# Performance work log

Hardware: AMD Instinct MI355X
Metric: run time of the kernel (lower is better)

## Reference

```python
import jax, jax.numpy as jnp
import numpy as np

NUM_FIELDS = 39
PER_FIELD_VOCAB = 10000
TOTAL_VOCAB = NUM_FIELDS * PER_FIELD_VOCAB
EMBED_DIM = 128
DIM_INT = (2, 3)
RANKS = (128, 128)
BATCH = 2048


def setup_inputs() -> dict:
    key = jax.random.key(0)
    k_x, k_emb, k_lin, k_b, k_w0, k_w1 = jax.random.split(key, 6)
    x = jax.random.randint(k_x, (BATCH, NUM_FIELDS), 0, PER_FIELD_VOCAB, dtype=jnp.int64 if jax.config.jax_enable_x64 else jnp.int32)
    embed_table = jax.random.normal(k_emb, (TOTAL_VOCAB, EMBED_DIM), dtype=jnp.float32) * 0.01
    linear_table = jax.random.normal(k_lin, (TOTAL_VOCAB, 1), dtype=jnp.float32) * 0.01
    bias = jnp.zeros((1,), dtype=jnp.float32)
    # trunc_normal_(std=0.01) approximated by scaled normal (same distribution family)
    W0 = jax.random.normal(k_w0, (DIM_INT[0], RANKS[0], NUM_FIELDS), dtype=jnp.float32) * 0.01
    W1 = jax.random.normal(k_w1, (DIM_INT[1], RANKS[1], NUM_FIELDS), dtype=jnp.float32) * 0.01
    return {"x": x, "embed_table": embed_table, "linear_table": linear_table,
            "bias": bias, "W0": W0, "W1": W1}


def _calc_cross(emb, W):
    # emb: [B, F, D]; W: [L, R, F]
    # dot_products[b,d,r,l] = sum_f W[l,r,f] * emb[b,f,d]   (torch: 'bljk,bki->bijl')
    dp = jnp.einsum('lrf,bfd->bdrl', W, emb)          # [B, D, R, L]
    prod_over_l = jnp.prod(dp, axis=3)                # [B, D, R]
    return jnp.sum(prod_over_l, axis=(1, 2))[:, None]  # [B, 1]


def reference(x, embed_table, linear_table, bias, W0, W1):
    # per-field offsets into the flat embedding table (FeaturesEmbedding behavior)
    offsets = (jnp.arange(NUM_FIELDS) * PER_FIELD_VOCAB).astype(x.dtype)
    idx = x + offsets[None, :]                        # [B, F]
    emb = embed_table[idx]                            # [B, F, D]
    # FeaturesLinear: sum of per-feature weights + bias -> [B, 1]
    ret = jnp.sum(linear_table[idx], axis=1) + bias
    for W in (W0, W1):
        ret = ret + _calc_cross(emb, W)
    return (ret, 0)
```

## Files before the change

kernel.cpp:

```cpp
#include <hip/hip_runtime.h>
#include <hip/hip_bf16.h>

#define NUM_FIELDS 39
#define PER_FIELD_VOCAB 10000
#define EMBED_DIM 128
#define KPAD 64
#define NL 5
#define RANK 128
#define BATCH 2048
#define LDS_STRIDE 72

typedef __bf16  bf16x8  __attribute__((ext_vector_type(8)));
typedef float   f32x4   __attribute__((ext_vector_type(4)));

__global__ __launch_bounds__(256) void prep_w(const float* __restrict__ W0,
                                              const float* __restrict__ W1,
                                              __bf16* __restrict__ Wb) {
    int i = blockIdx.x * 256 + threadIdx.x;
    if (i >= NL * RANK * KPAD) return;
    int f = i & (KPAD - 1);
    int r = (i >> 6) & (RANK - 1);
    int l = i >> 13;
    float v = 0.f;
    if (f < NUM_FIELDS) {
        if (l < 2) v = W0[(l * RANK + r) * NUM_FIELDS + f];
        else       v = W1[((l - 2) * RANK + r) * NUM_FIELDS + f];
    }
    Wb[i] = (__bf16)v;
}

__global__ __launch_bounds__(256) void tfm_main(const int* __restrict__ x,
                                                const float* __restrict__ embed_table,
                                                const float* __restrict__ linear_table,
                                                const float* __restrict__ bias,
                                                const __bf16* __restrict__ Wb,
                                                float* __restrict__ out,
                                                int out_size) {
    __shared__ int   sidx[NUM_FIELDS];
    __shared__ __align__(16) __bf16 eT[EMBED_DIM * LDS_STRIDE];
    __shared__ float wpart[4];

    const int tid = threadIdx.x;
    const int b   = blockIdx.x;

    if (tid < NUM_FIELDS)
        sidx[tid] = x[b * NUM_FIELDS + tid] + tid * PER_FIELD_VOCAB;
    __syncthreads();

    for (int k = tid; k < NUM_FIELDS * EMBED_DIM; k += 256) {
        int f = k >> 7, d = k & (EMBED_DIM - 1);
        float v = embed_table[(long)sidx[f] * EMBED_DIM + d];
        eT[d * LDS_STRIDE + f] = (__bf16)v;
    }
    for (int k = tid; k < (KPAD - NUM_FIELDS) * EMBED_DIM; k += 256) {
        int f = NUM_FIELDS + (k >> 7), d = k & (EMBED_DIM - 1);
        eT[d * LDS_STRIDE + f] = (__bf16)0.f;
    }

    float partial = 0.f;
    if (tid < NUM_FIELDS) partial = linear_table[sidx[tid]];

    __syncthreads();

    const int wave = tid >> 6, lane = tid & 63;
    const int m = lane & 15, quad = lane >> 4;

    for (int rti = 0; rti < 2; ++rti) {
        const int r0 = (wave * 2 + rti) * 16;
        bf16x8 afrag[NL][2];
#pragma unroll
        for (int l = 0; l < NL; ++l)
#pragma unroll
            for (int kc = 0; kc < 2; ++kc)
                afrag[l][kc] = *reinterpret_cast<const bf16x8*>(
                    &Wb[((size_t)(l * RANK) + r0 + m) * KPAD + kc * 32 + quad * 8]);

        for (int dt = 0; dt < 8; ++dt) {
            const int d0 = dt * 16;
            bf16x8 bfrag[2];
#pragma unroll
            for (int kc = 0; kc < 2; ++kc)
                bfrag[kc] = *reinterpret_cast<const bf16x8*>(
                    &eT[(d0 + m) * LDS_STRIDE + kc * 32 + quad * 8]);

            f32x4 acc[NL];
#pragma unroll
            for (int l = 0; l < NL; ++l) {
                acc[l] = (f32x4){0.f, 0.f, 0.f, 0.f};
#pragma unroll
                for (int kc = 0; kc < 2; ++kc)
                    acc[l] = __builtin_amdgcn_mfma_f32_16x16x32_bf16(
                        afrag[l][kc], bfrag[kc], acc[l], 0, 0, 0);
            }
#pragma unroll
            for (int i = 0; i < 4; ++i)
                partial += acc[0][i] * acc[1][i] + acc[2][i] * acc[3][i] * acc[4][i];
        }
    }

#pragma unroll
    for (int off = 32; off > 0; off >>= 1)
        partial += __shfl_down(partial, off, 64);
    if (lane == 0) wpart[wave] = partial;
    __syncthreads();
    if (tid == 0)
        out[b] = wpart[0] + wpart[1] + wpart[2] + wpart[3] + bias[0];

    if (b == 0)
        for (int j = BATCH + tid; j < out_size; j += 256)
            out[j] = 0.f;
}

extern "C" void kernel_launch(void* const* d_in, const int* in_sizes, int n_in,
                              void* d_out, int out_size, void* d_ws, size_t ws_size,
                              hipStream_t stream) {
    const int*   x            = (const int*)d_in[0];
    const float* embed_table  = (const float*)d_in[1];
    const float* linear_table = (const float*)d_in[2];
    const float* bias         = (const float*)d_in[3];
    const float* W0           = (const float*)d_in[4];
    const float* W1           = (const float*)d_in[5];
    __bf16*      Wb           = (__bf16*)d_ws;

    prep_w<<<(NL * RANK * KPAD + 255) / 256, 256, 0, stream>>>(W0, W1, Wb);
    tfm_main<<<BATCH, 256, 0, stream>>>(x, embed_table, linear_table, bias, Wb,
                                        (float*)d_out, out_size);
}
```

Before: 277.2 us.

## Replace order-2 cross term with Gram matrix contracted against precomputed W0 pair matrix

The L=2 cross term is rewritten algebraically: sum over d,r of the two projections equals the sum over field pairs of the embedding Gram matrix (E E^T) weighted by M01 = W0[0]^T W0[1]. The prep kernel now computes M01 once, and the main kernel builds the 48x48 Gram matrix per sample with MFMA instead of two rank-128 projection GEMMs. This removes 2 of the 5 projection MFMAs per tile. The cost is an extra row-major copy of the embeddings in LDS and per-lane global loads of M01.

```diff
diff --git a/kernel.cpp b/kernel.cpp
--- a/kernel.cpp
+++ b/kernel.cpp
@@ -5,28 +5,41 @@
 #define PER_FIELD_VOCAB 10000
 #define EMBED_DIM 128
 #define KPAD 64
-#define NL 5
+#define NT 3
 #define RANK 128
 #define BATCH 2048
-#define LDS_STRIDE 72
+#define ET_STRIDE 72
+#define E_STRIDE 144
+#define FPAD 48
 
 typedef __bf16  bf16x8  __attribute__((ext_vector_type(8)));
 typedef float   f32x4   __attribute__((ext_vector_type(4)));
 
-__global__ __launch_bounds__(256) void prep_w(const float* __restrict__ W0,
-                                              const float* __restrict__ W1,
-                                              __bf16* __restrict__ Wb) {
-    int i = blockIdx.x * 256 + threadIdx.x;
-    if (i >= NL * RANK * KPAD) return;
-    int f = i & (KPAD - 1);
-    int r = (i >> 6) & (RANK - 1);
-    int l = i >> 13;
-    float v = 0.f;
-    if (f < NUM_FIELDS) {
-        if (l < 2) v = W0[(l * RANK + r) * NUM_FIELDS + f];
-        else       v = W1[((l - 2) * RANK + r) * NUM_FIELDS + f];
+__global__ __launch_bounds__(256) void prep(const float* __restrict__ W0,
+                                            const float* __restrict__ W1,
+                                            __bf16* __restrict__ Wb,
+                                            float* __restrict__ M01) {
+    int blk = blockIdx.x;
+    if (blk < 96) {
+        int i = blk * 256 + threadIdx.x;
+        int f = i & (KPAD - 1);
+        int r = (i >> 6) & (RANK - 1);
+        int l = i >> 13;
+        float v = (f < NUM_FIELDS) ? W1[(l * RANK + r) * NUM_FIELDS + f] : 0.f;
+        Wb[i] = (__bf16)v;
+    } else {
+        int j = (blk - 96) * 256 + threadIdx.x;
+        if (j < FPAD * FPAD) {
+            int f0 = j / FPAD, f1 = j % FPAD;
+            float s = 0.f;
+            if (f0 < NUM_FIELDS && f1 < NUM_FIELDS) {
+#pragma unroll 8
+                for (int r = 0; r < RANK; ++r)
+                    s += W0[r * NUM_FIELDS + f0] * W0[(RANK + r) * NUM_FIELDS + f1];
+            }
+            M01[j] = s;
+        }
     }
-    Wb[i] = (__bf16)v;
 }
 
 __global__ __launch_bounds__(256) void tfm_main(const int* __restrict__ x,
@@ -34,10 +47,12 @@
                                                 const float* __restrict__ linear_table,
                                                 const float* __restrict__ bias,
                                                 const __bf16* __restrict__ Wb,
+                                                const float* __restrict__ M01,
                                                 float* __restrict__ out,
                                                 int out_size) {
     __shared__ int   sidx[NUM_FIELDS];
-    __shared__ __align__(16) __bf16 eT[EMBED_DIM * LDS_STRIDE];
+    __shared__ __align__(16) __bf16 eT[EMBED_DIM * ET_STRIDE];
+    __shared__ __align__(16) __bf16 e [FPAD * E_STRIDE];
     __shared__ float wpart[4];
 
     const int tid = threadIdx.x;
@@ -49,12 +64,18 @@
 
     for (int k = tid; k < NUM_FIELDS * EMBED_DIM; k += 256) {
         int f = k >> 7, d = k & (EMBED_DIM - 1);
-        float v = embed_table[(long)sidx[f] * EMBED_DIM + d];
-        eT[d * LDS_STRIDE + f] = (__bf16)v;
+        float v = embed_table[(size_t)sidx[f] * EMBED_DIM + d];
+        __bf16 bv = (__bf16)v;
+        eT[d * ET_STRIDE + f] = bv;
+        e [f * E_STRIDE  + d] = bv;
     }
     for (int k = tid; k < (KPAD - NUM_FIELDS) * EMBED_DIM; k += 256) {
         int f = NUM_FIELDS + (k >> 7), d = k & (EMBED_DIM - 1);
-        eT[d * LDS_STRIDE + f] = (__bf16)0.f;
+        eT[d * ET_STRIDE + f] = (__bf16)0.f;
+    }
+    for (int k = tid; k < (FPAD - NUM_FIELDS) * EMBED_DIM; k += 256) {
+        int f = NUM_FIELDS + (k >> 7), d = k & (EMBED_DIM - 1);
+        e[f * E_STRIDE + d] = (__bf16)0.f;
     }
 
     float partial = 0.f;
@@ -65,38 +86,60 @@
     const int wave = tid >> 6, lane = tid & 63;
     const int m = lane & 15, quad = lane >> 4;
 
+    bf16x8 afrag[2][NT][2];
+#pragma unroll
     for (int rti = 0; rti < 2; ++rti) {
         const int r0 = (wave * 2 + rti) * 16;
-        bf16x8 afrag[NL][2];
 #pragma unroll
-        for (int l = 0; l < NL; ++l)
+        for (int l = 0; l < NT; ++l)
 #pragma unroll
             for (int kc = 0; kc < 2; ++kc)
-                afrag[l][kc] = *reinterpret_cast<const bf16x8*>(
+                afrag[rti][l][kc] = *reinterpret_cast<const bf16x8*>(
                     &Wb[((size_t)(l * RANK) + r0 + m) * KPAD + kc * 32 + quad * 8]);
+    }
 
-        for (int dt = 0; dt < 8; ++dt) {
-            const int d0 = dt * 16;
-            bf16x8 bfrag[2];
+    float triplep = 0.f;
+    for (int dt = 0; dt < 8; ++dt) {
+        bf16x8 bfrag[2];
 #pragma unroll
-            for (int kc = 0; kc < 2; ++kc)
-                bfrag[kc] = *reinterpret_cast<const bf16x8*>(
-                    &eT[(d0 + m) * LDS_STRIDE + kc * 32 + quad * 8]);
-
-            f32x4 acc[NL];
+        for (int kc = 0; kc < 2; ++kc)
+            bfrag[kc] = *reinterpret_cast<const bf16x8*>(
+                &eT[(dt * 16 + m) * ET_STRIDE + kc * 32 + quad * 8]);
 #pragma unroll
-            for (int l = 0; l < NL; ++l) {
+        for (int rti = 0; rti < 2; ++rti) {
+            f32x4 acc[NT];
+#pragma unroll
+            for (int l = 0; l < NT; ++l) {
                 acc[l] = (f32x4){0.f, 0.f, 0.f, 0.f};
 #pragma unroll
                 for (int kc = 0; kc < 2; ++kc)
                     acc[l] = __builtin_amdgcn_mfma_f32_16x16x32_bf16(
-                        afrag[l][kc], bfrag[kc], acc[l], 0, 0, 0);
+                        afrag[rti][l][kc], bfrag[kc], acc[l], 0, 0, 0);
             }
 #pragma unroll
             for (int i = 0; i < 4; ++i)
-                partial += acc[0][i] * acc[1][i] + acc[2][i] * acc[3][i] * acc[4][i];
+                triplep += acc[0][i] * acc[1][i] * acc[2][i];
         }
     }
+
+    float pairp = 0.f;
+    for (int t = wave; t < 9; t += 4) {
+        const int ti = t / 3, tj = t % 3;
+        f32x4 g = (f32x4){0.f, 0.f, 0.f, 0.f};
+#pragma unroll
+        for (int kc = 0; kc < 4; ++kc) {
+            bf16x8 ga = *reinterpret_cast<const bf16x8*>(
+                &e[(ti * 16 + m) * E_STRIDE + kc * 32 + quad * 8]);
+            bf16x8 gb = *reinterpret_cast<const bf16x8*>(
+                &e[(tj * 16 + m) * E_STRIDE + kc * 32 + quad * 8]);
+            g = __builtin_amdgcn_mfma_f32_16x16x32_bf16(ga, gb, g, 0, 0, 0);
+        }
+#pragma unroll
+        for (int i = 0; i < 4; ++i)
+            pairp += g[i] * M01[(ti * 16 + quad * 4 + i) * FPAD + tj * 16 + m];
+    }
+
+    partial += triplep + pairp;
 
 #pragma unroll
     for (int off = 32; off > 0; off >>= 1)
@@ -120,9 +163,10 @@
     const float* bias         = (const float*)d_in[3];
     const float* W0           = (const float*)d_in[4];
     const float* W1           = (const float*)d_in[5];
-    __bf16*      Wb           = (__bf16*)d_ws;
+    __bf16* Wb  = (__bf16*)d_ws;
+    float*  M01 = (float*)((char*)d_ws + 49152);
 
-    prep_w<<<(NL * RANK * KPAD + 255) / 256, 256, 0, stream>>>(W0, W1, Wb);
-    tfm_main<<<BATCH, 256, 0, stream>>>(x, embed_table, linear_table, bias, Wb,
+    prep<<<96 + 9, 256, 0, stream>>>(W0, W1, Wb, M01);
+    tfm_main<<<BATCH, 256, 0, stream>>>(x, embed_table, linear_table, bias, Wb, M01,
                                         (float*)d_out, out_size);
 }
```

After: 311.2 us. 1.12x slower.

## Fuse weight conversion into main kernel and swizzle packed embedding LDS stores

Applied to the files above, without the earlier changes.

Removes the separate prep_w launch: each block now loads fp32 W0/W1 rows straight from global and converts them to bf16 fragments in registers. The embedding gather is restructured so each thread gathers four fields and writes a packed bf16x4 into an XOR-style swizzled LDS layout, which also zero-fills the padding in the same pass. The cross computation is split into separate W0 (pair) and W1 (triple) passes to lower register pressure, and launch bounds now request 6 blocks per CU. The cost is that every block repeats the weight conversion with unaligned scalar/vector loads instead of reading a precomputed bf16 buffer.

```diff
diff --git a/kernel.cpp b/kernel.cpp
--- a/kernel.cpp
+++ b/kernel.cpp
@@ -4,40 +4,44 @@
 #define NUM_FIELDS 39
 #define PER_FIELD_VOCAB 10000
 #define EMBED_DIM 128
-#define KPAD 64
-#define NL 5
 #define RANK 128
 #define BATCH 2048
-#define LDS_STRIDE 72
+#define ET_STRIDE 72
 
-typedef __bf16  bf16x8  __attribute__((ext_vector_type(8)));
-typedef float   f32x4   __attribute__((ext_vector_type(4)));
+typedef __bf16 bf16x8 __attribute__((ext_vector_type(8)));
+typedef __bf16 bf16x4 __attribute__((ext_vector_type(4)));
+typedef float  f32x4  __attribute__((ext_vector_type(4)));
+typedef float  f32x4u __attribute__((ext_vector_type(4), aligned(4)));
+typedef float  f32x2u __attribute__((ext_vector_type(2), aligned(4)));
 
-__global__ __launch_bounds__(256) void prep_w(const float* __restrict__ W0,
-                                              const float* __restrict__ W1,
-                                              __bf16* __restrict__ Wb) {
-    int i = blockIdx.x * 256 + threadIdx.x;
-    if (i >= NL * RANK * KPAD) return;
-    int f = i & (KPAD - 1);
-    int r = (i >> 6) & (RANK - 1);
-    int l = i >> 13;
-    float v = 0.f;
-    if (f < NUM_FIELDS) {
-        if (l < 2) v = W0[(l * RANK + r) * NUM_FIELDS + f];
-        else       v = W1[((l - 2) * RANK + r) * NUM_FIELDS + f];
+__device__ inline bf16x8 load_afrag(const float* __restrict__ Wrow, int quad, int kc) {
+    if (kc == 0) {
+        f32x4u a = *reinterpret_cast<const f32x4u*>(Wrow + quad * 8);
+        f32x4u b = *reinterpret_cast<const f32x4u*>(Wrow + quad * 8 + 4);
+        return (bf16x8){(__bf16)a[0], (__bf16)a[1], (__bf16)a[2], (__bf16)a[3],
+                        (__bf16)b[0], (__bf16)b[1], (__bf16)b[2], (__bf16)b[3]};
     }
-    Wb[i] = (__bf16)v;
+    if (quad == 0) {
+        f32x4u a = *reinterpret_cast<const f32x4u*>(Wrow + 32);
+        f32x2u b = *reinterpret_cast<const f32x2u*>(Wrow + 36);
+        float  c = Wrow[38];
+        return (bf16x8){(__bf16)a[0], (__bf16)a[1], (__bf16)a[2], (__bf16)a[3],
+                        (__bf16)b[0], (__bf16)b[1], (__bf16)c, (__bf16)0.f};
+    }
+    return (bf16x8){(__bf16)0.f, (__bf16)0.f, (__bf16)0.f, (__bf16)0.f,
+                    (__bf16)0.f, (__bf16)0.f, (__bf16)0.f, (__bf16)0.f};
 }
 
-__global__ __launch_bounds__(256) void tfm_main(const int* __restrict__ x,
-                                                const float* __restrict__ embed_table,
-                                                const float* __restrict__ linear_table,
-                                                const float* __restrict__ bias,
-                                                const __bf16* __restrict__ Wb,
-                                                float* __restrict__ out,
-                                                int out_size) {
-    __shared__ int   sidx[NUM_FIELDS];
-    __shared__ __align__(16) __bf16 eT[EMBED_DIM * LDS_STRIDE];
+__global__ __launch_bounds__(256, 6) void tfm_fused(const int* __restrict__ x,
+                                                    const float* __restrict__ embed_table,
+                                                    const float* __restrict__ linear_table,
+                                                    const float* __restrict__ bias,
+                                                    const float* __restrict__ W0,
+                                                    const float* __restrict__ W1,
+                                                    float* __restrict__ out,
+                                                    int out_size) {
+    __shared__ int sidx[NUM_FIELDS];
+    __shared__ __align__(16) __bf16 eT[EMBED_DIM * ET_STRIDE];
     __shared__ float wpart[4];
 
     const int tid = threadIdx.x;
@@ -47,56 +51,96 @@
         sidx[tid] = x[b * NUM_FIELDS + tid] + tid * PER_FIELD_VOCAB;
     __syncthreads();
 
-    for (int k = tid; k < NUM_FIELDS * EMBED_DIM; k += 256) {
-        int f = k >> 7, d = k & (EMBED_DIM - 1);
-        float v = embed_table[(long)sidx[f] * EMBED_DIM + d];
-        eT[d * LDS_STRIDE + f] = (__bf16)v;
-    }
-    for (int k = tid; k < (KPAD - NUM_FIELDS) * EMBED_DIM; k += 256) {
-        int f = NUM_FIELDS + (k >> 7), d = k & (EMBED_DIM - 1);
-        eT[d * LDS_STRIDE + f] = (__bf16)0.f;
+#pragma unroll
+    for (int i = 0; i < 8; ++i) {
+        int k  = tid + i * 256;
+        int d  = k & (EMBED_DIM - 1);
+        int fq = k >> 7;
+        float v[4];
+#pragma unroll
+        for (int c = 0; c < 4; ++c) {
+            int f = fq * 4 + c;
+            v[c] = (f < NUM_FIELDS) ? embed_table[(size_t)sidx[f] * EMBED_DIM + d] : 0.f;
+        }
+        bf16x4 pk = {(__bf16)v[0], (__bf16)v[1], (__bf16)v[2], (__bf16)v[3]};
+        int fg  = fq >> 1;
+        int grp = (fg + 2 * d) & 7;
+        *reinterpret_cast<bf16x4*>(reinterpret_cast<char*>(eT)
+            + d * (ET_STRIDE * 2) + grp * 16 + (fq & 1) * 8) = pk;
     }
 
-    float partial = 0.f;
-    if (tid < NUM_FIELDS) partial = linear_table[sidx[tid]];
-
+    float partial = (tid < NUM_FIELDS) ? linear_table[sidx[tid]] : 0.f;
     __syncthreads();
 
     const int wave = tid >> 6, lane = tid & 63;
     const int m = lane & 15, quad = lane >> 4;
 
+    float pairp = 0.f, trip = 0.f;
+
     for (int rti = 0; rti < 2; ++rti) {
-        const int r0 = (wave * 2 + rti) * 16;
-        bf16x8 afrag[NL][2];
+        const int r = (wave * 2 + rti) * 16 + m;
+
+        {
+            bf16x8 af[2][2];
 #pragma unroll
-        for (int l = 0; l < NL; ++l)
-#pragma unroll
-            for (int kc = 0; kc < 2; ++kc)
-                afrag[l][kc] = *reinterpret_cast<const bf16x8*>(
-                    &Wb[((size_t)(l * RANK) + r0 + m) * KPAD + kc * 32 + quad * 8]);
-
-        for (int dt = 0; dt < 8; ++dt) {
-            const int d0 = dt * 16;
-            bf16x8 bfrag[2];
-#pragma unroll
-            for (int kc = 0; kc < 2; ++kc)
-                bfrag[kc] = *reinterpret_cast<const bf16x8*>(
-                    &eT[(d0 + m) * LDS_STRIDE + kc * 32 + quad * 8]);
-
-            f32x4 acc[NL];
-#pragma unroll
-            for (int l = 0; l < NL; ++l) {
-                acc[l] = (f32x4){0.f, 0.f, 0.f, 0.f};
+            for (int l = 0; l < 2; ++l) {
+                const float* Wrow = W0 + ((size_t)(l * RANK) + r) * NUM_FIELDS;
 #pragma unroll
                 for (int kc = 0; kc < 2; ++kc)
-                    acc[l] = __builtin_amdgcn_mfma_f32_16x16x32_bf16(
-                        afrag[l][kc], bfrag[kc], acc[l], 0, 0, 0);
+                    af[l][kc] = load_afrag(Wrow, quad, kc);
             }
+            for (int dt = 0; dt < 8; ++dt) {
+                const int d = dt * 16 + m;
+                bf16x8 bfrag[2];
 #pragma unroll
-            for (int i = 0; i < 4; ++i)
-                partial += acc[0][i] * acc[1][i] + acc[2][i] * acc[3][i] * acc[4][i];
+                for (int kc = 0; kc < 2; ++kc) {
+                    int grp = ((kc * 4 + quad) + 2 * d) & 7;
+                    bfrag[kc] = *reinterpret_cast<const bf16x8*>(
+                        reinterpret_cast<const char*>(eT) + d * (ET_STRIDE * 2) + grp * 16);
+                }
+                f32x4 a0 = {0.f, 0.f, 0.f, 0.f}, a1 = {0.f, 0.f, 0.f, 0.f};
+#pragma unroll
+                for (int kc = 0; kc < 2; ++kc) {
+                    a0 = __builtin_amdgcn_mfma_f32_16x16x32_bf16(af[0][kc], bfrag[kc], a0, 0, 0, 0);
+                    a1 = __builtin_amdgcn_mfma_f32_16x16x32_bf16(af[1][kc], bfrag[kc], a1, 0, 0, 0);
+                }
+#pragma unroll
+                for (int i = 0; i < 4; ++i) pairp += a0[i] * a1[i];
+            }
+        }
+
+        {
+            bf16x8 ag[3][2];
+#pragma unroll
+            for (int l = 0; l < 3; ++l) {
+                const float* Wrow = W1 + ((size_t)(l * RANK) + r) * NUM_FIELDS;
+#pragma unroll
+                for (int kc = 0; kc < 2; ++kc)
+                    ag[l][kc] = load_afrag(Wrow, quad, kc);
+            }
+            for (int dt = 0; dt < 8; ++dt) {
+                const int d = dt * 16 + m;
+                bf16x8 bfrag[2];
+#pragma unroll
+                for (int kc = 0; kc < 2; ++kc) {
+                    int grp = ((kc * 4 + quad) + 2 * d) & 7;
+                    bfrag[kc] = *reinterpret_cast<const bf16x8*>(
+                        reinterpret_cast<const char*>(eT) + d * (ET_STRIDE * 2) + grp * 16);
+                }
+                f32x4 a2 = {0.f, 0.f, 0.f, 0.f}, a3 = {0.f, 0.f, 0.f, 0.f}, a4 = {0.f, 0.f, 0.f, 0.f};
+#pragma unroll
+                for (int kc = 0; kc < 2; ++kc) {
+                    a2 = __builtin_amdgcn_mfma_f32_16x16x32_bf16(ag[0][kc], bfrag[kc], a2, 0, 0, 0);
+                    a3 = __builtin_amdgcn_mfma_f32_16x16x32_bf16(ag[1][kc], bfrag[kc], a3, 0, 0, 0);
+                    a4 = __builtin_amdgcn_mfma_f32_16x16x32_bf16(ag[2][kc], bfrag[kc], a4, 0, 0, 0);
+                }
+#pragma unroll
+                for (int i = 0; i < 4; ++i) trip += a2[i] * a3[i] * a4[i];
+            }
         }
     }
+
+    partial += pairp + trip;
 
 #pragma unroll
     for (int off = 32; off > 0; off >>= 1)
@@ -120,9 +164,7 @@
     const float* bias         = (const float*)d_in[3];
     const float* W0           = (const float*)d_in[4];
     const float* W1           = (const float*)d_in[5];
-    __bf16*      Wb           = (__bf16*)d_ws;
 
-    prep_w<<<(NL * RANK * KPAD + 255) / 256, 256, 0, stream>>>(W0, W1, Wb);
-    tfm_main<<<BATCH, 256, 0, stream>>>(x, embed_table, linear_table, bias, Wb,
-                                        (float*)d_out, out_size);
+    tfm_fused<<<BATCH, 256, 0, stream>>>(x, embed_table, linear_table, bias, W0, W1,
+                                         (float*)d_out, out_size);
 }
```

Measured after the change: 488.2 us. 76.1% more time.

## Swizzle transposed embedding LDS layout and pack four fields per store

Applied to the files above, without the earlier changes.

Rewrites the gather-and-transpose into LDS so each thread loads four fields for one embedding dimension and writes them as a packed bf16x4, with an XOR-style group swizzle on the row layout to avoid bank conflicts, and folds the zero padding into the same loop. The MFMA loop is reordered so the five independent accumulators interleave across k-chunks, and the pair and triple products go into separate accumulators. The aim is to cut LDS store count and bank conflicts in the staging phase and expose more MFMA independence, at the cost of more complex index math.

```diff
diff --git a/kernel.cpp b/kernel.cpp
--- a/kernel.cpp
+++ b/kernel.cpp
@@ -8,10 +8,11 @@
 #define NL 5
 #define RANK 128
 #define BATCH 2048
-#define LDS_STRIDE 72
+#define ET_ROW 144
 
-typedef __bf16  bf16x8  __attribute__((ext_vector_type(8)));
-typedef float   f32x4   __attribute__((ext_vector_type(4)));
+typedef __bf16 bf16x8 __attribute__((ext_vector_type(8)));
+typedef __bf16 bf16x4 __attribute__((ext_vector_type(4)));
+typedef float  f32x4  __attribute__((ext_vector_type(4)));
 
 __global__ __launch_bounds__(256) void prep_w(const float* __restrict__ W0,
                                               const float* __restrict__ W1,
@@ -36,8 +37,8 @@
                                                 const __bf16* __restrict__ Wb,
                                                 float* __restrict__ out,
                                                 int out_size) {
-    __shared__ int   sidx[NUM_FIELDS];
-    __shared__ __align__(16) __bf16 eT[EMBED_DIM * LDS_STRIDE];
+    __shared__ int sidx[NUM_FIELDS];
+    __shared__ __align__(16) char eT[EMBED_DIM * ET_ROW];
     __shared__ float wpart[4];
 
     const int tid = threadIdx.x;
@@ -47,56 +48,68 @@
         sidx[tid] = x[b * NUM_FIELDS + tid] + tid * PER_FIELD_VOCAB;
     __syncthreads();
 
-    for (int k = tid; k < NUM_FIELDS * EMBED_DIM; k += 256) {
-        int f = k >> 7, d = k & (EMBED_DIM - 1);
-        float v = embed_table[(long)sidx[f] * EMBED_DIM + d];
-        eT[d * LDS_STRIDE + f] = (__bf16)v;
-    }
-    for (int k = tid; k < (KPAD - NUM_FIELDS) * EMBED_DIM; k += 256) {
-        int f = NUM_FIELDS + (k >> 7), d = k & (EMBED_DIM - 1);
-        eT[d * LDS_STRIDE + f] = (__bf16)0.f;
+#pragma unroll
+    for (int i = 0; i < 8; ++i) {
+        int k  = tid + i * 256;
+        int d  = k & (EMBED_DIM - 1);
+        int fq = k >> 7;
+        float v[4];
+#pragma unroll
+        for (int c = 0; c < 4; ++c) {
+            int f = fq * 4 + c;
+            v[c] = (f < NUM_FIELDS) ? embed_table[(size_t)sidx[f] * EMBED_DIM + d] : 0.f;
+        }
+        bf16x4 pk = {(__bf16)v[0], (__bf16)v[1], (__bf16)v[2], (__bf16)v[3]};
+        int fg  = fq >> 1;
+        int grp = (fg + 2 * d) & 7;
+        *reinterpret_cast<bf16x4*>(eT + d * ET_ROW + grp * 16 + (fq & 1) * 8) = pk;
     }
 
-    float partial = 0.f;
-    if (tid < NUM_FIELDS) partial = linear_table[sidx[tid]];
-
+    float partial = (tid < NUM_FIELDS) ? linear_table[sidx[tid]] : 0.f;
     __syncthreads();
 
     const int wave = tid >> 6, lane = tid & 63;
     const int m = lane & 15, quad = lane >> 4;
 
+    float pairp = 0.f, trip = 0.f;
+
     for (int rti = 0; rti < 2; ++rti) {
-        const int r0 = (wave * 2 + rti) * 16;
-        bf16x8 afrag[NL][2];
+        const int r = (wave * 2 + rti) * 16 + m;
+
+        bf16x8 af[NL][2];
 #pragma unroll
         for (int l = 0; l < NL; ++l)
 #pragma unroll
             for (int kc = 0; kc < 2; ++kc)
-                afrag[l][kc] = *reinterpret_cast<const bf16x8*>(
-                    &Wb[((size_t)(l * RANK) + r0 + m) * KPAD + kc * 32 + quad * 8]);
+                af[l][kc] = *reinterpret_cast<const bf16x8*>(
+                    &Wb[((size_t)(l * RANK) + r) * KPAD + kc * 32 + quad * 8]);
 
         for (int dt = 0; dt < 8; ++dt) {
-            const int d0 = dt * 16;
+            const int d = dt * 16 + m;
             bf16x8 bfrag[2];
 #pragma unroll
-            for (int kc = 0; kc < 2; ++kc)
-                bfrag[kc] = *reinterpret_cast<const bf16x8*>(
-                    &eT[(d0 + m) * LDS_STRIDE + kc * 32 + quad * 8]);
-
+            for (int kc = 0; kc < 2; ++kc) {
+                int grp = ((kc * 4 + quad) + 2 * d) & 7;
+                bfrag[kc] = *reinterpret_cast<const bf16x8*>(eT + d * ET_ROW + grp * 16);
+            }
             f32x4 acc[NL];
 #pragma unroll
-            for (int l = 0; l < NL; ++l) {
-                acc[l] = (f32x4){0.f, 0.f, 0.f, 0.f};
+            for (int l = 0; l < NL; ++l) acc[l] = (f32x4){0.f, 0.f, 0.f, 0.f};
 #pragma unroll
-                for (int kc = 0; kc < 2; ++kc)
+            for (int kc = 0; kc < 2; ++kc)
+#pragma unroll
+                for (int l = 0; l < NL; ++l)
                     acc[l] = __builtin_amdgcn_mfma_f32_16x16x32_bf16(
-                        afrag[l][kc], bfrag[kc], acc[l], 0, 0, 0);
+                        af[l][kc], bfrag[kc], acc[l], 0, 0, 0);
+#pragma unroll
+            for (int i = 0; i < 4; ++i) {
+                pairp += acc[0][i] * acc[1][i];
+                trip  += acc[2][i] * acc[3][i] * acc[4][i];
             }
-#pragma unroll
-            for (int i = 0; i < 4; ++i)
-                partial += acc[0][i] * acc[1][i] + acc[2][i] * acc[3][i] * acc[4][i];
         }
     }
+
+    partial += pairp + trip;
 
 #pragma unroll
     for (int off = 32; off > 0; off >>= 1)
@@ -120,7 +133,7 @@
     const float* bias         = (const float*)d_in[3];
     const float* W0           = (const float*)d_in[4];
     const float* W1           = (const float*)d_in[5];
-    __bf16*      Wb           = (__bf16*)d_ws;
+    __bf16* Wb = (__bf16*)d_ws;
 
     prep_w<<<(NL * RANK * KPAD + 255) / 256, 256, 0, stream>>>(W0, W1, Wb);
     tfm_main<<<BATCH, 256, 0, stream>>>(x, embed_table, linear_table, bias, Wb,
```

Measured after the change: 287.6 us. +3.8%, slower.
